# Kernel tuning notes

Measured on AMD Instinct MI355X. Metric: run time of the kernel, lower is better.

Reference implementation:

```python
import jax, jax.numpy as jnp
import numpy as np

V, T, D, L, H, F = 32000, 1024, 768, 8, 12, 3072
DH = D // H
SCALE = 1.0 / np.sqrt(DH)
EPS = 1e-5


def layer_norm(x, w, b):
    mu = jnp.mean(x, axis=-1, keepdims=True)
    var = jnp.mean(jnp.square(x - mu), axis=-1, keepdims=True)
    return (x - mu) * jax.lax.rsqrt(var + EPS) * w + b


def setup_inputs() -> dict:
    key = jax.random.key(0)
    ks = jax.random.split(key, 10)
    def nrm(k, shape, std=0.02):
        return (jax.random.normal(k, shape, dtype=jnp.float32) * std)
    inp = {
        "idx": jax.random.randint(ks[0], (4, T), 0, V, dtype=jnp.int32),
        "targets": jax.random.randint(ks[1], (4, T), 0, V, dtype=jnp.int32),
        "tok_emb": nrm(ks[2], (V, D)),
        "pos_emb": nrm(ks[3], (T, D)),
        "qkv_w": nrm(ks[4], (L, 3 * D, D)),
        "qkv_b": jnp.zeros((L, 3 * D), jnp.float32),
        "proj_w": nrm(ks[5], (L, D, D)),
        "proj_b": jnp.zeros((L, D), jnp.float32),
        "fc1_w": nrm(ks[6], (L, F, D)),
        "fc1_b": jnp.zeros((L, F), jnp.float32),
        "fc2_w": nrm(ks[7], (L, D, F)),
        "fc2_b": jnp.zeros((L, D), jnp.float32),
        "ln1_w": jnp.ones((L, D), jnp.float32),
        "ln1_b": jnp.zeros((L, D), jnp.float32),
        "ln2_w": jnp.ones((L, D), jnp.float32),
        "ln2_b": jnp.zeros((L, D), jnp.float32),
        "lnf_w": jnp.ones((D,), jnp.float32),
        "lnf_b": jnp.zeros((D,), jnp.float32),
    }
    return inp


def gpt_forward(idx, targets, tok_emb, pos_emb, qkv_w, qkv_b, proj_w, proj_b,
                fc1_w, fc1_b, fc2_w, fc2_b, ln1_w, ln1_b, ln2_w, ln2_b, lnf_w, lnf_b):
    B, Tc = idx.shape
    x = tok_emb[idx] + pos_emb[:Tc][None]  # [B,T,D]
    causal = jnp.tril(jnp.ones((Tc, Tc), bool))

    def block(x, p):
        qw, qb, pw, pb, f1w, f1b, f2w, f2b, l1w, l1b, l2w, l2b = p
        h = layer_norm(x, l1w, l1b)
        qkv = h @ qw.T + qb  # [B,T,3D]
        q, k, v = jnp.split(qkv, 3, axis=-1)
        q = q.reshape(B, Tc, H, DH).transpose(0, 2, 1, 3)  # [B,H,T,DH]
        k = k.reshape(B, Tc, H, DH).transpose(0, 2, 1, 3)
        v = v.reshape(B, Tc, H, DH).transpose(0, 2, 1, 3)
        att = jnp.einsum('bhqd,bhkd->bhqk', q, k) * SCALE
        att = jnp.where(causal, att, -jnp.inf)
        att = jax.nn.softmax(att, axis=-1)
        y = jnp.einsum('bhqk,bhkd->bhqd', att, v)
        y = y.transpose(0, 2, 1, 3).reshape(B, Tc, D)
        x = x + y @ pw.T + pb
        h2 = layer_norm(x, l2w, l2b)
        x = x + jax.nn.gelu(h2 @ f1w.T + f1b, approximate=False) @ f2w.T + f2b
        return x, None

    x, _ = jax.lax.scan(block, x, (qkv_w, qkv_b, proj_w, proj_b,
                                   fc1_w, fc1_b, fc2_w, fc2_b,
                                   ln1_w, ln1_b, ln2_w, ln2_b))
    x = layer_norm(x, lnf_w, lnf_b)
    logits = jnp.einsum('btd,vd->btv', x, tok_emb)  # tied lm_head, output_mult=1
    logp = jax.nn.log_softmax(logits, axis=-1)
    valid = targets != -100
    tgt = jnp.where(valid, targets, 0)
    nll = -jnp.take_along_axis(logp, tgt[..., None], axis=-1)[..., 0]
    loss = jnp.sum(nll * valid) / jnp.maximum(jnp.sum(valid), 1)
    return logits, loss


def reference(idx, targets, tok_emb, pos_emb, qkv_w, qkv_b, proj_w, proj_b,
              fc1_w, fc1_b, fc2_w, fc2_b, ln1_w, ln1_b, ln2_w, ln2_b, lnf_w, lnf_b):
    return gpt_forward(idx, targets, tok_emb, pos_emb, qkv_w, qkv_b, proj_w, proj_b,
                       fc1_w, fc1_b, fc2_w, fc2_b, ln1_w, ln1_b, ln2_w, ln2_b, lnf_w, lnf_b)
```

## Files before the change

kernel.cpp:

```cpp
#include <hip/hip_runtime.h>
#include <hip/hip_bf16.h>
#include <math.h>

#define BATCH 4
#define T 1024
#define D 768
#define L 8
#define H 12
#define F 3072
#define V 32000
#define DH 64
#define M (BATCH*T)
#define D3 (3*D)
#define SCALE 0.125f
#define VCHUNK 6400
#define PBT 125

typedef unsigned short u16;
typedef __attribute__((ext_vector_type(8))) short bf16x8;
typedef __attribute__((ext_vector_type(4))) float f32x4;

__device__ inline u16 f2b(float f) {
  __hip_bfloat16 h = __float2bfloat16(f);
  return *(u16*)&h;
}

__device__ inline void gll16(const void* g, void* l) {
  __builtin_amdgcn_global_load_lds(
      (const __attribute__((address_space(1))) unsigned int*)g,
      (__attribute__((address_space(3))) unsigned int*)l, 16, 0, 0);
}

__device__ inline int swzi(int r, int c) {
  return (r * 64 + c) ^ ((((r & 7) ^ ((r >> 3) & 7))) << 3);
}

__device__ inline float block_reduce(float v, bool is_max, float* buf4) {
  int lane = threadIdx.x & 63, wid = threadIdx.x >> 6;
#pragma unroll
  for (int off = 32; off; off >>= 1) {
    float o = __shfl_down(v, off, 64);
    v = is_max ? fmaxf(v, o) : v + o;
  }
  if (lane == 0) buf4[wid] = v;
  __syncthreads();
  float r = is_max ? fmaxf(fmaxf(buf4[0], buf4[1]), fmaxf(buf4[2], buf4[3]))
                   : buf4[0] + buf4[1] + buf4[2] + buf4[3];
  __syncthreads();
  return r;
}

__global__ __launch_bounds__(256) void k_embed(const int* __restrict__ idx,
                                               const float* __restrict__ tok,
                                               const float* __restrict__ pos,
                                               float* __restrict__ x) {
  int i = blockIdx.x * 256 + threadIdx.x;
  int row = i / D, d = i - row * D;
  int t = row & (T - 1);
  x[i] = tok[(size_t)idx[row] * D + d] + pos[(size_t)t * D + d];
}

__global__ __launch_bounds__(256) void k_cvt(const float* __restrict__ in,
                                             u16* __restrict__ out, int n4) {
  int i = blockIdx.x * 256 + threadIdx.x;
  if (i >= n4) return;
  float4 v = ((const float4*)in)[i];
  ushort4 o;
  o.x = f2b(v.x); o.y = f2b(v.y); o.z = f2b(v.z); o.w = f2b(v.w);
  ((ushort4*)out)[i] = o;
}

__global__ __launch_bounds__(256) void k_cvtw(const float* __restrict__ q,
                                              const float* __restrict__ p,
                                              const float* __restrict__ f1,
                                              const float* __restrict__ f2,
                                              u16* __restrict__ out) {
  const int N0 = L * D3 * D / 4, N1 = L * D * D / 4;
  const int N2 = L * F * D / 4, N3 = L * D * F / 4;
  int i = blockIdx.x * 256 + threadIdx.x;
  if (i >= N0 + N1 + N2 + N3) return;
  const float* src;
  int j = i;
  if (i < N0) { src = q; }
  else if (i < N0 + N1) { src = p; j = i - N0; }
  else if (i < N0 + N1 + N2) { src = f1; j = i - N0 - N1; }
  else { src = f2; j = i - N0 - N1 - N2; }
  float4 v = ((const float4*)src)[j];
  ushort4 o;
  o.x = f2b(v.x); o.y = f2b(v.y); o.z = f2b(v.z); o.w = f2b(v.w);
  ((ushort4*)out)[i] = o;
}

__global__ __launch_bounds__(256) void k_lnorm(const float* __restrict__ x,
                                               const float* __restrict__ w,
                                               const float* __restrict__ b,
                                               u16* __restrict__ out) {
  int lane = threadIdx.x & 63, wid = threadIdx.x >> 6;
  int row = blockIdx.x * 4 + wid;
  const float4* xr = (const float4*)(x + (size_t)row * D);
  float4 v[3];
  float s = 0.f, ss = 0.f;
#pragma unroll
  for (int p = 0; p < 3; ++p) {
    v[p] = xr[lane + 64 * p];
    s += v[p].x + v[p].y + v[p].z + v[p].w;
    ss += v[p].x * v[p].x + v[p].y * v[p].y + v[p].z * v[p].z + v[p].w * v[p].w;
  }
#pragma unroll
  for (int off = 32; off; off >>= 1) {
    s += __shfl_xor(s, off, 64);
    ss += __shfl_xor(ss, off, 64);
  }
  float mu = s * (1.0f / D);
  float var = ss * (1.0f / D) - mu * mu;
  float rs = rsqrtf(var + 1e-5f);
  ushort4* orow = (ushort4*)(out + (size_t)row * D);
#pragma unroll
  for (int p = 0; p < 3; ++p) {
    float4 wv = ((const float4*)w)[lane + 64 * p];
    float4 bv = ((const float4*)b)[lane + 64 * p];
    ushort4 o;
    o.x = f2b((v[p].x - mu) * rs * wv.x + bv.x);
    o.y = f2b((v[p].y - mu) * rs * wv.y + bv.y);
    o.z = f2b((v[p].z - mu) * rs * wv.z + bv.z);
    o.w = f2b((v[p].w - mu) * rs * wv.w + bv.w);
    orow[lane + 64 * p] = o;
  }
}

__global__ __launch_bounds__(512, 2) void k_gemm8(
    const u16* __restrict__ A, const u16* __restrict__ W,
    const float* __restrict__ bias, const float* __restrict__ resid,
    void* __restrict__ Cout, int K, int ldC, int flags) {
  __shared__ __attribute__((aligned(16))) u16 lds[2][2][128 * 64];
  int tid = threadIdx.x, w = tid >> 6, lane = tid & 63;
  int wm = w >> 2, wn = w & 3;
  int bn = blockIdx.x, bm = blockIdx.y;
  int frow = lane & 15, g = lane >> 4;
  int sr = lane >> 3, scu = lane & 7;
  const u16* Ab = A + (size_t)bm * 128 * K;
  const u16* Wb = W + (size_t)bn * 128 * K;
  int NT = K >> 6;

  f32x4 acc[4][2];
#pragma unroll
  for (int i = 0; i < 4; ++i)
#pragma unroll
    for (int j = 0; j < 2; ++j) acc[i][j] = (f32x4)(0.f);

#define STG(t)                                                            \
  {                                                                       \
    _Pragma("unroll") for (int rr = 0; rr < 2; ++rr) {                    \
      int row = rr * 64 + w * 8 + sr;                                     \
      int gcu = scu ^ (row & 7);                                          \
      gll16(Ab + (size_t)row * K + (t) * 64 + gcu * 8,                    \
            &lds[(t) & 1][0][(rr * 64 + w * 8) * 64]);                    \
      gll16(Wb + (size_t)row * K + (t) * 64 + gcu * 8,                    \
            &lds[(t) & 1][1][(rr * 64 + w * 8) * 64]);                    \
    }                                                                     \
  }

  STG(0);
  asm volatile("s_waitcnt vmcnt(0)");
  __builtin_amdgcn_s_barrier();

  for (int t = 0; t < NT; ++t) {
    if (t + 1 < NT) {
      STG(t + 1);
      asm volatile("s_waitcnt vmcnt(4)");
    } else {
      asm volatile("s_waitcnt vmcnt(0)");
    }
    __builtin_amdgcn_s_barrier();
    const u16* bA = &lds[t & 1][0][0];
    const u16* bB = &lds[t & 1][1][0];
    bf16x8 ar[8], br[4];
#pragma unroll
    for (int i = 0; i < 4; ++i)
#pragma unroll
      for (int kk = 0; kk < 2; ++kk) {
        int r = wm * 64 + i * 16 + frow;
        ar[i * 2 + kk] = *(const bf16x8*)(bA + r * 64 + ((g + kk * 4) ^ (r & 7)) * 8);
      }
#pragma unroll
    for (int j = 0; j < 2; ++j)
#pragma unroll
      for (int kk = 0; kk < 2; ++kk) {
        int r = wn * 32 + j * 16 + frow;
        br[j * 2 + kk] = *(const bf16x8*)(bB + r * 64 + ((g + kk * 4) ^ (r & 7)) * 8);
      }
    __builtin_amdgcn_s_setprio(1);
#pragma unroll
    for (int i = 0; i < 4; ++i)
#pragma unroll
      for (int j = 0; j < 2; ++j)
#pragma unroll
        for (int kk = 0; kk < 2; ++kk)
          acc[i][j] = __builtin_amdgcn_mfma_f32_16x16x32_bf16(
              ar[i * 2 + kk], br[j * 2 + kk], acc[i][j], 0, 0, 0);
    __builtin_amdgcn_s_setprio(0);
    __builtin_amdgcn_s_barrier();
  }
#undef STG

  int m0 = bm * 128 + wm * 64 + g * 4;
  int n0 = bn * 128 + wn * 32 + frow;
#pragma unroll
  for (int i = 0; i < 4; ++i) {
#pragma unroll
    for (int j = 0; j < 2; ++j) {
      int n = n0 + j * 16;
      float bv = (flags & 1) ? bias[n] : 0.f;
#pragma unroll
      for (int q = 0; q < 4; ++q) {
        int m = m0 + i * 16 + q;
        size_t off = (size_t)m * ldC + n;
        float v = acc[i][j][q] + bv;
        if (flags & 4) v = 0.5f * v * (1.0f + erff(v * 0.70710678118f));
        if (flags & 2) v += resid[off];
        if (flags & 8) ((u16*)Cout)[off] = f2b(v);
        else           ((float*)Cout)[off] = v;
      }
    }
  }
}

__global__ __launch_bounds__(512, 2) void k_lm256(
    const u16* __restrict__ A,
    const u16* __restrict__ B,
    float* __restrict__ C,
    float* __restrict__ pm, float* __restrict__ ps,
    int gc0) {
  __shared__ __attribute__((aligned(16))) u16 lds[2][2][2][128 * 64];
  __shared__ float pml[256][4], psl[256][4];
  const int K = 768, NT = 12;
  int tid = threadIdx.x, w = tid >> 6, lane = tid & 63;
  int wm = w >> 2, wn = w & 3;
  int bm = blockIdx.y, bn = blockIdx.x;
  int frow = lane & 15, g = lane >> 4;
  int sr = lane >> 3, scu = lane & 7;
  const u16* Abase = A + (size_t)bm * 256 * K;
  const u16* Bbase = B + (size_t)bn * 256 * K;

  f32x4 acc[8][4];
#pragma unroll
  for (int i = 0; i < 8; ++i)
#pragma unroll
    for (int j = 0; j < 4; ++j) acc[i][j] = (f32x4)(0.f);

#define STAGE(t, h)                                                       \
  {                                                                       \
    const u16* src = ((h) < 2 ? Abase : Bbase) + (size_t)(((h)&1) * 128) * K; \
    u16* dst = &lds[(t) & 1][(h) >> 1][(h)&1][0];                         \
    _Pragma("unroll") for (int rr = 0; rr < 2; ++rr) {                    \
      int row = rr * 64 + w * 8 + sr;                                     \
      int gcu = scu ^ (row & 7);                                          \
      gll16(src + (size_t)row * K + (t) * 64 + gcu * 8,                   \
            dst + (rr * 64 + w * 8) * 64);                                \
    }                                                                     \
  }

  bf16x8 ar[8], br[8];
#define LDA(T_, ILO)                                                      \
  {                                                                       \
    const u16* base = &lds[(T_)&1][0][wm][0];                             \
    _Pragma("unroll") for (int ii = 0; ii < 4; ++ii)                      \
    _Pragma("unroll") for (int kk = 0; kk < 2; ++kk) {                    \
      int ri = ((ILO) + ii) * 16 + frow;                                  \
      int u = (g + kk * 4) ^ (ri & 7);                                    \
      ar[ii * 2 + kk] = *(const bf16x8*)(base + ri * 64 + u * 8);         \
    }                                                                     \
  }
#define LDB(T_, JLO, BO)                                                  \
  {                                                                       \
    const u16* base = &lds[(T_)&1][1][wn >> 1][0];                        \
    _Pragma("unroll") for (int jj = 0; jj < 2; ++jj)                      \
    _Pragma("unroll") for (int kk = 0; kk < 2; ++kk) {                    \
      int rj = (wn & 1) * 64 + ((JLO) + jj) * 16 + frow;                  \
      int u = (g + kk * 4) ^ (rj & 7);                                    \
      br[(BO) + jj * 2 + kk] = *(const bf16x8*)(base + rj * 64 + u * 8);  \
    }                                                                     \
  }
#define MFMA16(ILO, JLO, BO)                                              \
  _Pragma("unroll") for (int ii = 0; ii < 4; ++ii)                        \
  _Pragma("unroll") for (int jj = 0; jj < 2; ++jj)                        \
  _Pragma("unroll") for (int kk = 0; kk < 2; ++kk)                        \
    acc[(ILO) + ii][(JLO) + jj] = __builtin_amdgcn_mfma_f32_16x16x32_bf16( \
        ar[ii * 2 + kk], br[(BO) + jj * 2 + kk], acc[(ILO) + ii][(JLO) + jj], 0, 0, 0);

  STAGE(0, 0); STAGE(0, 1); STAGE(0, 2); STAGE(0, 3);
  asm volatile("s_waitcnt vmcnt(0)");
  __builtin_amdgcn_s_barrier();

  for (int t = 0; t < NT; ++t) {
    bool pf = (t + 1 < NT);
    LDA(t, 0); LDB(t, 0, 0);
    if (pf) { STAGE(t + 1, 0); STAGE(t + 1, 1); }
    __builtin_amdgcn_s_setprio(1);
    MFMA16(0, 0, 0);
    __builtin_amdgcn_s_setprio(0);
    __builtin_amdgcn_s_barrier();
    LDB(t, 2, 4);
    if (pf) { STAGE(t + 1, 2); STAGE(t + 1, 3); }
    __builtin_amdgcn_s_setprio(1);
    MFMA16(0, 2, 4);
    __builtin_amdgcn_s_setprio(0);
    __builtin_amdgcn_s_barrier();
    LDA(t, 4);
    __builtin_amdgcn_s_setprio(1);
    MFMA16(4, 2, 4);
    __builtin_amdgcn_s_setprio(0);
    __builtin_amdgcn_s_barrier();
    __builtin_amdgcn_s_setprio(1);
    MFMA16(4, 0, 0);
    __builtin_amdgcn_s_setprio(0);
    asm volatile("s_waitcnt vmcnt(0)");
    __builtin_amdgcn_s_barrier();
  }

#pragma unroll
  for (int ii = 0; ii < 8; ++ii) {
#pragma unroll
    for (int q = 0; q < 4; ++q) {
      float mx = fmaxf(fmaxf(acc[ii][0][q], acc[ii][1][q]),
                       fmaxf(acc[ii][2][q], acc[ii][3][q]));
      mx = fmaxf(mx, __shfl_xor(mx, 1, 64));
      mx = fmaxf(mx, __shfl_xor(mx, 2, 64));
      mx = fmaxf(mx, __shfl_xor(mx, 4, 64));
      mx = fmaxf(mx, __shfl_xor(mx, 8, 64));
      float sm = 0.f;
#pragma unroll
      for (int jj = 0; jj < 4; ++jj) sm += __expf(acc[ii][jj][q] - mx);
      sm += __shfl_xor(sm, 1, 64);
      sm += __shfl_xor(sm, 2, 64);
      sm += __shfl_xor(sm, 4, 64);
      sm += __shfl_xor(sm, 8, 64);
      int lrow = wm * 128 + ii * 16 + g * 4 + q;
      if (frow == 0) { pml[lrow][wn] = mx; psl[lrow][wn] = sm; }
      size_t off = (size_t)(bm * 256 + lrow) * V + gc0 + bn * 256 + wn * 64 + frow;
#pragma unroll
      for (int jj = 0; jj < 4; ++jj) C[off + jj * 16] = acc[ii][jj][q];
    }
  }
  __syncthreads();
  if (tid < 256) {
    float m = fmaxf(fmaxf(pml[tid][0], pml[tid][1]), fmaxf(pml[tid][2], pml[tid][3]));
    float s = 0.f;
#pragma unroll
    for (int w4 = 0; w4 < 4; ++w4) s += psl[tid][w4] * __expf(pml[tid][w4] - m);
    size_t grow = bm * 256 + tid;
    int pb = gc0 / 256 + bn;
    pm[grow * PBT + pb] = m;
    ps[grow * PBT + pb] = s;
  }
#undef STAGE
#undef LDA
#undef LDB
#undef MFMA16
}

__global__ __launch_bounds__(512) void k_fattn(const u16* __restrict__ qkv,
                                               u16* __restrict__ y) {
  __shared__ __attribute__((aligned(16))) u16 lQ[2][64 * 64];
  __shared__ __attribute__((aligned(16))) u16 lK[64 * 64];
  __shared__ __attribute__((aligned(16))) u16 lVt[64 * 64];
  __shared__ __attribute__((aligned(16))) u16 lP[128 * 64];
  int tid = threadIdx.x;
  int w = tid >> 6, lane = tid & 63;
  int tq = w >> 2, ws4 = w & 3;
  int xi = blockIdx.x;
  int bh = blockIdx.y, b = bh / H, h = bh - b * H;
  int myqt = tq ? xi : (15 - xi);
  const u16* base = qkv + (size_t)b * T * D3 + h * DH;
  int srow = lane >> 3;
  int scu = lane & 7;
  int frow = lane & 15, g = lane >> 4;
  int s16 = ws4 * 16;
  int qrow = g * 4;
  int f7 = frow & 7;

#pragma unroll
  for (int c = 0; c < 2; ++c) {
    int row = s16 + c * 8 + srow;
    int gcu = scu ^ (row & 7);
    gll16(base + (size_t)(myqt * 64 + row) * D3 + gcu * 8,
          &lQ[tq][(s16 + c * 8) * 64]);
  }

  float m_r[4], l_r[4];
  f32x4 o[4];
#pragma unroll
  for (int i = 0; i < 4; ++i) { m_r[i] = -1e30f; l_r[i] = 0.f; o[i] = (f32x4)(0.f); }

  int ktmax = 15 - xi;
  int kvrow = w * 8 + srow;
  uint4 kr = *(const uint4*)(base + D + (size_t)kvrow * D3 + scu * 8);
  uint4 vr = *(const uint4*)(base + 2 * D + (size_t)kvrow * D3 + scu * 8);

  for (int kt = 0; kt <= ktmax; ++kt) {
    __syncthreads();
    int k0 = kt * 64;
    *(uint4*)(lK + kvrow * 64 + (scu ^ (kvrow & 7)) * 8) = kr;
    {
      unsigned vals[4] = {vr.x, vr.y, vr.z, vr.w};
#pragma unroll
      for (int e = 0; e < 4; ++e) {
        lVt[swzi(scu * 8 + 2 * e, kvrow)]     = (u16)(vals[e] & 0xffff);
        lVt[swzi(scu * 8 + 2 * e + 1, kvrow)] = (u16)(vals[e] >> 16);
      }
    }
    __syncthreads();
    if (kt < ktmax) {
      int rown = k0 + 64 + kvrow;
      kr = *(const uint4*)(base + D + (size_t)rown * D3 + scu * 8);
      vr = *(const uint4*)(base + 2 * D + (size_t)rown * D3 + scu * 8);
    }

    if (tq == 0 || kt <= xi) {
      bool diag = (kt == myqt);
      const u16* lq = &lQ[tq][0];
      bf16x8 aq0 = *(const bf16x8*)(lq + (s16 + frow) * 64 + (g ^ f7) * 8);
      bf16x8 aq1 = *(const bf16x8*)(lq + (s16 + frow) * 64 + ((g + 4) ^ f7) * 8);
      f32x4 sv[4];
#pragma unroll
      for (int kn = 0; kn < 4; ++kn) {
        bf16x8 bk0 = *(const bf16x8*)(lK + (kn * 16 + frow) * 64 + (g ^ f7) * 8);
        bf16x8 bk1 = *(const bf16x8*)(lK + (kn * 16 + frow) * 64 + ((g + 4) ^ f7) * 8);
        sv[kn] = __builtin_amdgcn_mfma_f32_16x16x32_bf16(aq0, bk0, (f32x4)(0.f), 0, 0, 0);
        sv[kn] = __builtin_amdgcn_mfma_f32_16x16x32_bf16(aq1, bk1, sv[kn], 0, 0, 0);
      }
#pragma unroll
      for (int kn = 0; kn < 4; ++kn)
#pragma unroll
        for (int qi = 0; qi < 4; ++qi) {
          float v = sv[kn][qi] * SCALE;
          if (diag) {
            int qg = myqt * 64 + s16 + qrow + qi;
            int kg = k0 + kn * 16 + frow;
            if (kg > qg) v = -1e30f;
          }
          sv[kn][qi] = v;
        }
#pragma unroll
      for (int qi = 0; qi < 4; ++qi) {
        float rm = fmaxf(fmaxf(sv[0][qi], sv[1][qi]), fmaxf(sv[2][qi], sv[3][qi]));
        rm = fmaxf(rm, __shfl_xor(rm, 1, 64));
        rm = fmaxf(rm, __shfl_xor(rm, 2, 64));
        rm = fmaxf(rm, __shfl_xor(rm, 4, 64));
        rm = fmaxf(rm, __shfl_xor(rm, 8, 64));
        float mn = fmaxf(m_r[qi], rm);
        float alpha = __expf(m_r[qi] - mn);
        m_r[qi] = mn;
        float rs = 0.f;
#pragma unroll
        for (int kn = 0; kn < 4; ++kn) {
          float p = __expf(sv[kn][qi] - mn);
          sv[kn][qi] = p;
          rs += p;
        }
        rs += __shfl_xor(rs, 1, 64);
        rs += __shfl_xor(rs, 2, 64);
        rs += __shfl_xor(rs, 4, 64);
        rs += __shfl_xor(rs, 8, 64);
        l_r[qi] = l_r[qi] * alpha + rs;
#pragma unroll
        for (int df = 0; df < 4; ++df) o[df][qi] *= alpha;
      }
#pragma unroll
      for (int kn = 0; kn < 4; ++kn)
#pragma unroll
        for (int qi = 0; qi < 4; ++qi)
          lP[swzi(w * 16 + qrow + qi, kn * 16 + frow)] = f2b(sv[kn][qi]);
      bf16x8 pa0 = *(const bf16x8*)(lP + swzi(w * 16 + frow, g * 8));
      bf16x8 pa1 = *(const bf16x8*)(lP + swzi(w * 16 + frow, 32 + g * 8));
#pragma unroll
      for (int df = 0; df < 4; ++df) {
        bf16x8 bv0 = *(const bf16x8*)(lVt + swzi(df * 16 + frow, g * 8));
        bf16x8 bv1 = *(const bf16x8*)(lVt + swzi(df * 16 + frow, 32 + g * 8));
        o[df] = __builtin_amdgcn_mfma_f32_16x16x32_bf16(pa0, bv0, o[df], 0, 0, 0);
        o[df] = __builtin_amdgcn_mfma_f32_16x16x32_bf16(pa1, bv1, o[df], 0, 0, 0);
      }
    }
  }

#pragma unroll
  for (int df = 0; df < 4; ++df)
#pragma unroll
    for (int qi = 0; qi < 4; ++qi) {
      int qg = myqt * 64 + s16 + qrow + qi;
      y[(size_t)(b * T + qg) * D + h * DH + df * 16 + frow] =
          f2b(o[df][qi] / l_r[qi]);
    }
}

__global__ __launch_bounds__(256) void k_loss_rows(
    const float* __restrict__ pm, const float* __restrict__ ps,
    const float* __restrict__ logits, const int* __restrict__ targets,
    float* __restrict__ nll) {
  int lane = threadIdx.x & 63, wid = threadIdx.x >> 6;
  int row = blockIdx.x * 4 + wid;
  const float* pmr = pm + (size_t)row * PBT;
  const float* psr = ps + (size_t)row * PBT;
  float m = -1e30f;
  for (int i = lane; i < PBT; i += 64) m = fmaxf(m, pmr[i]);
#pragma unroll
  for (int off = 32; off; off >>= 1) m = fmaxf(m, __shfl_xor(m, off, 64));
  float s = 0.f;
  for (int i = lane; i < PBT; i += 64) s += psr[i] * __expf(pmr[i] - m);
#pragma unroll
  for (int off = 32; off; off >>= 1) s += __shfl_xor(s, off, 64);
  if (lane == 0) {
    int tgt = targets[row];
    nll[row] = (tgt != -100) ? (m + logf(s) - logits[(size_t)row * V + tgt]) : 0.f;
  }
}

__global__ __launch_bounds__(256) void k_loss_final(const float* __restrict__ nll,
                                                    const int* __restrict__ targets,
                                                    float* __restrict__ out) {
  __shared__ float buf4[4];
  float s = 0.f, c = 0.f;
  for (int i = threadIdx.x; i < M; i += 256) {
    s += nll[i];
    c += (targets[i] != -100) ? 1.f : 0.f;
  }
  s = block_reduce(s, false, buf4);
  c = block_reduce(c, false, buf4);
  if (threadIdx.x == 0) out[0] = s / fmaxf(c, 1.f);
}

extern "C" void kernel_launch(void* const* d_in, const int* in_sizes, int n_in,
                              void* d_out, int out_size, void* d_ws, size_t ws_size,
                              hipStream_t stream) {
  const int* idx       = (const int*)d_in[0];
  const int* targets   = (const int*)d_in[1];
  const float* tok     = (const float*)d_in[2];
  const float* pos     = (const float*)d_in[3];
  const float* qkv_w   = (const float*)d_in[4];
  const float* qkv_b   = (const float*)d_in[5];
  const float* proj_w  = (const float*)d_in[6];
  const float* proj_b  = (const float*)d_in[7];
  const float* fc1_w   = (const float*)d_in[8];
  const float* fc1_b   = (const float*)d_in[9];
  const float* fc2_w   = (const float*)d_in[10];
  const float* fc2_b   = (const float*)d_in[11];
  const float* ln1_w   = (const float*)d_in[12];
  const float* ln1_b   = (const float*)d_in[13];
  const float* ln2_w   = (const float*)d_in[14];
  const float* ln2_b   = (const float*)d_in[15];
  const float* lnf_w   = (const float*)d_in[16];
  const float* lnf_b   = (const float*)d_in[17];

  float* logits = (float*)d_out;

  char* ws = (char*)d_ws;
  float* x   = (float*)ws;
  u16* hb    = (u16*)(ws + 12582912);
  u16* yb    = (u16*)(ws + 18874368);
  u16* wb    = (u16*)(ws + 25165824);
  bool big = ws_size >= (size_t)(25165824 + 49152000 + 2048000 * 2 + 16384);
  float* pm, * ps, * nll;
  if (big) {
    pm  = (float*)(ws + 25165824 + 49152000);
    ps  = (float*)(ws + 25165824 + 49152000 + 2048000);
    nll = (float*)(ws + 25165824 + 49152000 + 4096000);
  } else {
    pm  = (float*)(ws + 34996224);
    ps  = (float*)(ws + 37044224);
    nll = (float*)(ws + 39092224);
  }

  u16* qkvb   = (u16*)logits;
  u16* f1b    = (u16*)(logits + 9437184);
  u16* wqkv   = (u16*)(logits + 15728640);
  u16* wproj  = (u16*)(logits + 22806528);
  u16* wfc1   = (u16*)(logits + 25165824);
  u16* wfc2   = (u16*)(logits + 34603008);

  {
    const int NW4 = (L * D3 * D + L * D * D + L * F * D + L * D * F) / 4;
    k_cvtw<<<(NW4 + 255) / 256, 256, 0, stream>>>(qkv_w, proj_w, fc1_w, fc2_w, wqkv);
  }

  k_embed<<<(M * D) / 256, 256, 0, stream>>>(idx, tok, pos, x);

  for (int l = 0; l < L; ++l) {
    k_lnorm<<<M / 4, 256, 0, stream>>>(x, ln1_w + (size_t)l * D, ln1_b + (size_t)l * D, hb);
    k_gemm8<<<dim3(D3 / 128, M / 128), 512, 0, stream>>>(
        hb, wqkv + (size_t)l * D3 * D, qkv_b + (size_t)l * D3, nullptr, qkvb, D, D3, 9);
    k_fattn<<<dim3(8, BATCH * H), 512, 0, stream>>>(qkvb, yb);
    k_gemm8<<<dim3(D / 128, M / 128), 512, 0, stream>>>(
        yb, wproj + (size_t)l * D * D, proj_b + (size_t)l * D, x, x, D, D, 3);
    k_lnorm<<<M / 4, 256, 0, stream>>>(x, ln2_w + (size_t)l * D, ln2_b + (size_t)l * D, hb);
    k_gemm8<<<dim3(F / 128, M / 128), 512, 0, stream>>>(
        hb, wfc1 + (size_t)l * F * D, fc1_b + (size_t)l * F, nullptr, f1b, D, F, 13);
    k_gemm8<<<dim3(D / 128, M / 128), 512, 0, stream>>>(
        f1b, wfc2 + (size_t)l * D * F, fc2_b + (size_t)l * D, x, x, F, D, 3);
  }

  k_lnorm<<<M / 4, 256, 0, stream>>>(x, lnf_w, lnf_b, hb);
  if (big) {
    k_cvt<<<(V * D / 4 + 255) / 256, 256, 0, stream>>>(tok, wb, V * D / 4);
    k_lm256<<<dim3(V / 256, M / 256), 512, 0, stream>>>(
        hb, wb, logits, pm, ps, 0);
  } else {
    for (int c = 0; c < 5; ++c) {
      k_cvt<<<(VCHUNK * D / 4 + 255) / 256, 256, 0, stream>>>(
          tok + (size_t)c * VCHUNK * D, wb, VCHUNK * D / 4);
      k_lm256<<<dim3(VCHUNK / 256, M / 256), 512, 0, stream>>>(
          hb, wb, logits, pm, ps, c * VCHUNK);
    }
  }
  k_loss_rows<<<M / 4, 256, 0, stream>>>(pm, ps, logits, targets, nll);
  k_loss_final<<<1, 256, 0, stream>>>(nll, targets, logits + (size_t)M * V);
}
```

Baseline: 1.899 ms.

## Split-K the fc2 GEMM four ways and fuse partial reduction into next layernorm

The fc2 GEMM (K=3072, N=768) launched only 6x32 blocks, which underfills the GPU. It is now split four ways along K via blockIdx.z, and each slice writes fp32 partials to a scratch area inside the logits buffer. A new k_lncomb kernel sums the four partials with the bias and residual, writes x back, and applies the following layernorm in the same pass. This adds partial-buffer traffic and depends on the logits region at that offset being free during the transformer layers.

```diff
diff --git a/kernel.cpp b/kernel.cpp
--- a/kernel.cpp
+++ b/kernel.cpp
@@ -128,19 +128,68 @@
   }
 }
 
+__global__ __launch_bounds__(256) void k_lncomb(float* __restrict__ x,
+                                                const float* __restrict__ parts,
+                                                const float* __restrict__ bias2,
+                                                const float* __restrict__ w,
+                                                const float* __restrict__ b,
+                                                u16* __restrict__ out) {
+  int lane = threadIdx.x & 63, wid = threadIdx.x >> 6;
+  int row = blockIdx.x * 4 + wid;
+  float4* xr = (float4*)(x + (size_t)row * D);
+  float4 v[3];
+  float s = 0.f, ss = 0.f;
+#pragma unroll
+  for (int p = 0; p < 3; ++p) {
+    v[p] = xr[lane + 64 * p];
+#pragma unroll
+    for (int pp = 0; pp < 4; ++pp) {
+      float4 pv = ((const float4*)(parts + (size_t)pp * M * D + (size_t)row * D))[lane + 64 * p];
+      v[p].x += pv.x; v[p].y += pv.y; v[p].z += pv.z; v[p].w += pv.w;
+    }
+    float4 b2 = ((const float4*)bias2)[lane + 64 * p];
+    v[p].x += b2.x; v[p].y += b2.y; v[p].z += b2.z; v[p].w += b2.w;
+    s += v[p].x + v[p].y + v[p].z + v[p].w;
+    ss += v[p].x * v[p].x + v[p].y * v[p].y + v[p].z * v[p].z + v[p].w * v[p].w;
+  }
+#pragma unroll
+  for (int off = 32; off; off >>= 1) {
+    s += __shfl_xor(s, off, 64);
+    ss += __shfl_xor(ss, off, 64);
+  }
+  float mu = s * (1.0f / D);
+  float var = ss * (1.0f / D) - mu * mu;
+  float rs = rsqrtf(var + 1e-5f);
+  ushort4* orow = (ushort4*)(out + (size_t)row * D);
+#pragma unroll
+  for (int p = 0; p < 3; ++p) {
+    xr[lane + 64 * p] = v[p];
+    float4 wv = ((const float4*)w)[lane + 64 * p];
+    float4 bv = ((const float4*)b)[lane + 64 * p];
+    ushort4 o;
+    o.x = f2b((v[p].x - mu) * rs * wv.x + bv.x);
+    o.y = f2b((v[p].y - mu) * rs * wv.y + bv.y);
+    o.z = f2b((v[p].z - mu) * rs * wv.z + bv.z);
+    o.w = f2b((v[p].w - mu) * rs * wv.w + bv.w);
+    orow[lane + 64 * p] = o;
+  }
+}
+
 __global__ __launch_bounds__(512, 2) void k_gemm8(
     const u16* __restrict__ A, const u16* __restrict__ W,
     const float* __restrict__ bias, const float* __restrict__ resid,
-    void* __restrict__ Cout, int K, int ldC, int flags) {
+    void* __restrict__ Cout, int kLen, int kStride, int ldC, int flags) {
   __shared__ __attribute__((aligned(16))) u16 lds[2][2][128 * 64];
   int tid = threadIdx.x, w = tid >> 6, lane = tid & 63;
   int wm = w >> 2, wn = w & 3;
   int bn = blockIdx.x, bm = blockIdx.y;
   int frow = lane & 15, g = lane >> 4;
   int sr = lane >> 3, scu = lane & 7;
-  const u16* Ab = A + (size_t)bm * 128 * K;
-  const u16* Wb = W + (size_t)bn * 128 * K;
-  int NT = K >> 6;
+  int kz = (flags & 16) ? blockIdx.z * kLen : 0;
+  const u16* Ab = A + (size_t)bm * 128 * kStride + kz;
+  const u16* Wb = W + (size_t)bn * 128 * kStride + kz;
+  float* Cp = (float*)Cout + ((flags & 16) ? (size_t)blockIdx.z * M * (size_t)ldC : 0);
+  int NT = kLen >> 6;
 
   f32x4 acc[4][2];
 #pragma unroll
@@ -153,9 +202,9 @@
     _Pragma("unroll") for (int rr = 0; rr < 2; ++rr) {                    \
       int row = rr * 64 + w * 8 + sr;                                     \
       int gcu = scu ^ (row & 7);                                          \
-      gll16(Ab + (size_t)row * K + (t) * 64 + gcu * 8,                    \
+      gll16(Ab + (size_t)row * kStride + (t) * 64 + gcu * 8,              \
             &lds[(t) & 1][0][(rr * 64 + w * 8) * 64]);                    \
-      gll16(Wb + (size_t)row * K + (t) * 64 + gcu * 8,                    \
+      gll16(Wb + (size_t)row * kStride + (t) * 64 + gcu * 8,              \
             &lds[(t) & 1][1][(rr * 64 + w * 8) * 64]);                    \
     }                                                                     \
   }
@@ -219,17 +268,15 @@
         if (flags & 4) v = 0.5f * v * (1.0f + erff(v * 0.70710678118f));
         if (flags & 2) v += resid[off];
         if (flags & 8) ((u16*)Cout)[off] = f2b(v);
-        else           ((float*)Cout)[off] = v;
+        else           Cp[off] = v;
       }
     }
   }
 }
 
 __global__ __launch_bounds__(512, 2) void k_lm256(
-    const u16* __restrict__ A,
-    const u16* __restrict__ B,
-    float* __restrict__ C,
-    float* __restrict__ pm, float* __restrict__ ps,
+    const u16* __restrict__ A, const u16* __restrict__ B,
+    float* __restrict__ C, float* __restrict__ pm, float* __restrict__ ps,
     int gc0) {
   __shared__ __attribute__((aligned(16))) u16 lds[2][2][2][128 * 64];
   __shared__ float pml[256][4], psl[256][4];
@@ -576,6 +623,7 @@
   u16* wproj  = (u16*)(logits + 22806528);
   u16* wfc1   = (u16*)(logits + 25165824);
   u16* wfc2   = (u16*)(logits + 34603008);
+  float* fc2p = (float*)((char*)logits + 201326592);
 
   {
     const int NW4 = (L * D3 * D + L * D * D + L * F * D + L * D * F) / 4;
@@ -585,20 +633,25 @@
   k_embed<<<(M * D) / 256, 256, 0, stream>>>(idx, tok, pos, x);
 
   for (int l = 0; l < L; ++l) {
-    k_lnorm<<<M / 4, 256, 0, stream>>>(x, ln1_w + (size_t)l * D, ln1_b + (size_t)l * D, hb);
+    if (l == 0)
+      k_lnorm<<<M / 4, 256, 0, stream>>>(x, ln1_w, ln1_b, hb);
+    else
+      k_lncomb<<<M / 4, 256, 0, stream>>>(x, fc2p, fc2_b + (size_t)(l - 1) * D,
+                                          ln1_w + (size_t)l * D, ln1_b + (size_t)l * D, hb);
     k_gemm8<<<dim3(D3 / 128, M / 128), 512, 0, stream>>>(
-        hb, wqkv + (size_t)l * D3 * D, qkv_b + (size_t)l * D3, nullptr, qkvb, D, D3, 9);
+        hb, wqkv + (size_t)l * D3 * D, qkv_b + (size_t)l * D3, nullptr, qkvb, D, D, D3, 9);
     k_fattn<<<dim3(8, BATCH * H), 512, 0, stream>>>(qkvb, yb);
     k_gemm8<<<dim3(D / 128, M / 128), 512, 0, stream>>>(
-        yb, wproj + (size_t)l * D * D, proj_b + (size_t)l * D, x, x, D, D, 3);
+        yb, wproj + (size_t)l * D * D, proj_b + (size_t)l * D, x, x, D, D, D, 3);
     k_lnorm<<<M / 4, 256, 0, stream>>>(x, ln2_w + (size_t)l * D, ln2_b + (size_t)l * D, hb);
     k_gemm8<<<dim3(F / 128, M / 128), 512, 0, stream>>>(
-        hb, wfc1 + (size_t)l * F * D, fc1_b + (size_t)l * F, nullptr, f1b, D, F, 13);
-    k_gemm8<<<dim3(D / 128, M / 128), 512, 0, stream>>>(
-        f1b, wfc2 + (size_t)l * D * F, fc2_b + (size_t)l * D, x, x, F, D, 3);
-  }
-
-  k_lnorm<<<M / 4, 256, 0, stream>>>(x, lnf_w, lnf_b, hb);
+        hb, wfc1 + (size_t)l * F * D, fc1_b + (size_t)l * F, nullptr, f1b, D, D, F, 13);
+    k_gemm8<<<dim3(D / 128, M / 128, 4), 512, 0, stream>>>(
+        f1b, wfc2 + (size_t)l * D * F, nullptr, nullptr, fc2p, 768, F, D, 16);
+  }
+
+  k_lncomb<<<M / 4, 256, 0, stream>>>(x, fc2p, fc2_b + (size_t)(L - 1) * D,
+                                      lnf_w, lnf_b, hb);
   if (big) {
     k_cvt<<<(V * D / 4 + 255) / 256, 256, 0, stream>>>(tok, wb, V * D / 4);
     k_lm256<<<dim3(V / 256, M / 256), 512, 0, stream>>>(
```

After: 1.896 ms (median of 2 runs). About the same (-0.2%).
